# Kernel tuning notes

Measured on AMD Instinct MI355X. Metric: run time of the kernel, lower is better.

## Reference

```python
import jax, jax.numpy as jnp
import numpy as np

NUM_HEADS = 4
LOCAL_RADIUS = 2


def setup_inputs() -> dict:
    key = jax.random.key(0)
    ks = jax.random.split(key, 7)
    B, C, H, W = 1, 256, 40, 40
    O = 256  # out_channels
    s = 1.0 / np.sqrt(C).astype(np.float32)
    x = jax.random.normal(ks[0], (B, C, H, W), dtype=jnp.float32)
    Wq = jax.random.normal(ks[1], (C, O), dtype=jnp.float32) * s
    Wk = jax.random.normal(ks[2], (C, O), dtype=jnp.float32) * s
    Wv = jax.random.normal(ks[3], (C, O), dtype=jnp.float32) * s
    bq = jnp.zeros((O,), jnp.float32)
    bk = jnp.zeros((O,), jnp.float32)
    bv = jnp.zeros((O,), jnp.float32)
    return {"x": x, "Wq": Wq, "bq": bq, "Wk": Wk, "bk": bk, "Wv": Wv, "bv": bv}


def reference(x, Wq, bq, Wk, bk, Wv, bv):
    B, C, H, W = x.shape
    N = H * W
    O = Wq.shape[1]
    hd = O // NUM_HEADS
    # Faithful to torch: x.view(B, N, -1) is a raw row-major reshape of (B,C,H,W)
    xf = x.reshape(B, N, C)
    # projections -> (B, heads, N, head_dim)
    q = (xf @ Wq + bq).reshape(B, N, NUM_HEADS, hd).transpose(0, 2, 1, 3)
    k = (xf @ Wk + bk).reshape(B, N, NUM_HEADS, hd).transpose(0, 2, 1, 3)
    v = (xf @ Wv + bv).reshape(B, N, NUM_HEADS, hd).transpose(0, 2, 1, 3)
    scale = jnp.asarray(O, jnp.float32) ** 0.5
    acc = jnp.zeros_like(v)
    # 25 shifted full-attention passes; roll is over (heads, points) axes,
    # exactly matching torch key.roll(shifts=(h,w), dims=(-3,-2)).
    for h in range(-LOCAL_RADIUS, LOCAL_RADIUS + 1):
        for w in range(-LOCAL_RADIUS, LOCAL_RADIUS + 1):
            rk = jnp.roll(k, shift=(h, w), axis=(1, 2))
            scores = jnp.einsum('bhnd,bhmd->bhnm', q, rk) / scale  # (B,h,N,N)
            attn = jax.nn.softmax(scores, axis=-1)
            rv = jnp.roll(v, shift=(-h, -w), axis=(1, 2))
            acc = acc + jnp.einsum('bhnm,bhmd->bhnd', attn, rv)
    # (B, heads, N, hd) -> (B, N, O)
    return acc.transpose(0, 2, 1, 3).reshape(B, N, O)
```

## Files before the change

### kernel.cpp

```cpp
#include <hip/hip_runtime.h>
#include <hip/hip_bf16.h>
#include <stdint.h>

typedef __attribute__((ext_vector_type(8))) __bf16 bf16x8;
typedef __attribute__((ext_vector_type(4))) float f32x4;

#define N_PTS 1600
#define HD    64

#define OFF_WT   0u
#define OFF_BIAS 393216u
#define OFF_XS   394752u
#define OFF_QH   1213952u
#define OFF_KF   2033152u
#define OFF_VF   2852352u

__device__ __forceinline__ float bf2f(ushort h) {
  union { uint32_t u; float f; } v; v.u = ((uint32_t)h) << 16; return v.f;
}
__device__ __forceinline__ ushort f2bf(float f) {
  union { float f; uint32_t u; } v; v.f = f;
  uint32_t u = v.u;
  return (ushort)((u + 0x7FFFu + ((u >> 16) & 1u)) >> 16);
}
__device__ __forceinline__ uint32_t pk2(float a, float b) {
  union { __hip_bfloat162 h; uint32_t u; } cv;
  cv.h = __float22bfloat162_rn(make_float2(a, b));
  return cv.u;
}

__device__ __forceinline__ int detect_f32(const ushort* xu, int* shflag) {
  int t = threadIdx.x & 255;
  if (t == 0) *shflag = 0;
  __syncthreads();
  int local = 0;
#pragma unroll
  for (int i = 0; i < 4; ++i) {
    float v = bf2f(xu[(t * 4 + i) * 2]);
    if (!(fabsf(v) < 1e4f)) local = 1;
  }
  if (local) atomicOr(shflag, 1);
  __syncthreads();
  return *shflag;
}

__global__ void k_prep(const void* __restrict__ x, const void* __restrict__ Wq,
                       const void* __restrict__ bq, const void* __restrict__ Wk,
                       const void* __restrict__ bk, const void* __restrict__ Wv,
                       const void* __restrict__ bv, char* __restrict__ ws) {
  __shared__ int shflag;
  __shared__ ushort tileb[32][33];
  int isf32 = detect_f32((const ushort*)x, &shflag);
  int b = blockIdx.x, t = threadIdx.x;

  if (b < 192) {
    int z = b >> 6, tile = b & 63;
    const void* W = (z == 0) ? Wq : ((z == 1) ? Wk : Wv);
    int o0 = (tile & 7) * 32, k0 = (tile >> 3) * 32;
    int tx = t & 31, ty = t >> 5;
#pragma unroll
    for (int i = 0; i < 32; i += 8) {
      int kk = (k0 + ty + i) * 256 + o0 + tx;
      tileb[ty + i][tx] = isf32 ? f2bf(((const float*)W)[kk]) : ((const ushort*)W)[kk];
    }
    __syncthreads();
    ushort* WT = (ushort*)(ws + OFF_WT) + z * 65536;
#pragma unroll
    for (int i = 0; i < 32; i += 8)
      WT[(o0 + ty + i) * 256 + k0 + tx] = tileb[tx][ty + i];
  } else if (b == 192) {
    ushort* bb = (ushort*)(ws + OFF_BIAS);
#pragma unroll
    for (int z = 0; z < 3; ++z) {
      const void* B = (z == 0) ? bq : ((z == 1) ? bk : bv);
      bb[z * 256 + t] = isf32 ? f2bf(((const float*)B)[t]) : ((const ushort*)B)[t];
    }
  } else {
    int jid = (b - 193) * 256 + t;
    int n = jid >> 5, ch0 = (jid & 31) * 8;
    int nm4 = n - 4 + ((n < 4) ? 1600 : 0);
    int nm2 = n - 2 + ((n < 2) ? 1600 : 0);
    int np2 = n + 2 - ((n >= 1598) ? 1600 : 0);
    int np4 = n + 4 - ((n >= 1596) ? 1600 : 0);
    int rows[5] = {nm4, nm2, n, np2, np4};
    union { ushort us[8]; bf16x8 v; } rv[5];
    if (isf32) {
      const float4* X4 = (const float4*)x;
#pragma unroll
      for (int r = 0; r < 5; ++r) {
        int i4 = (rows[r] * 256 + ch0) >> 2;
        float4 f0 = X4[i4], f1 = X4[i4 + 1];
        rv[r].us[0] = f2bf(f0.x); rv[r].us[1] = f2bf(f0.y);
        rv[r].us[2] = f2bf(f0.z); rv[r].us[3] = f2bf(f0.w);
        rv[r].us[4] = f2bf(f1.x); rv[r].us[5] = f2bf(f1.y);
        rv[r].us[6] = f2bf(f1.z); rv[r].us[7] = f2bf(f1.w);
      }
    } else {
      const ushort* Xu = (const ushort*)x;
#pragma unroll
      for (int r = 0; r < 5; ++r)
        rv[r].v = *(const bf16x8*)(Xu + rows[r] * 256 + ch0);
    }
    union { ushort us[8]; bf16x8 v; } o;
#pragma unroll
    for (int j = 0; j < 8; ++j) {
      float s = bf2f(rv[0].us[j]) + bf2f(rv[1].us[j]) + bf2f(rv[2].us[j]) +
                bf2f(rv[3].us[j]) + bf2f(rv[4].us[j]);
      o.us[j] = f2bf(s);
    }
    *(bf16x8*)((ushort*)(ws + OFF_XS) + n * 256 + ch0) = o.v;
  }
}

__launch_bounds__(512)
__global__ void k_proj(const void* __restrict__ x, const ushort* __restrict__ WT,
                       const ushort* __restrict__ bias3, char* __restrict__ ws) {
  __shared__ int shflag;
  __shared__ ushort ktile[2][4][16][72];
  int isf32 = detect_f32((const ushort*)x, &shflag);
  int tid = threadIdx.x;
  int half = tid >> 8;
  int job = blockIdx.x + 150 * half;
  int z = job / 100, nb = job % 100;
  int n0 = nb * 16;
  const ushort* WTz = WT + z * 65536;
  const ushort* bias = bias3 + z * 256;
  int t256 = tid & 255;
  int head = t256 >> 6, lane = t256 & 63;
  int c = lane & 15, quad = lane >> 4;

  f32x4 acc[4];
#pragma unroll
  for (int i = 0; i < 4; ++i) acc[i] = (f32x4){0.f, 0.f, 0.f, 0.f};

  int ebase = (n0 + c) * 256;
  const ushort* Xs = (const ushort*)(ws + OFF_XS);
#pragma unroll
  for (int kt = 0; kt < 8; ++kt) {
    bf16x8 a;
    if (z == 2) {
      a = *(const bf16x8*)(Xs + ebase + kt * 32 + quad * 8);
    } else if (isf32) {
      const float4* X4 = (const float4*)x;
      int i4 = (ebase + kt * 32 + quad * 8) >> 2;
      float4 f0 = X4[i4], f1 = X4[i4 + 1];
      union { ushort us[8]; bf16x8 v; } cv;
      cv.us[0] = f2bf(f0.x); cv.us[1] = f2bf(f0.y);
      cv.us[2] = f2bf(f0.z); cv.us[3] = f2bf(f0.w);
      cv.us[4] = f2bf(f1.x); cv.us[5] = f2bf(f1.y);
      cv.us[6] = f2bf(f1.z); cv.us[7] = f2bf(f1.w);
      a = cv.v;
    } else {
      a = *(const bf16x8*)((const ushort*)x + ebase + kt * 32 + quad * 8);
    }
#pragma unroll
    for (int os = 0; os < 4; ++os) {
      bf16x8 bfr = *(const bf16x8*)(WTz + (head * 64 + os * 16 + c) * 256 + kt * 32 + quad * 8);
      acc[os] = __builtin_amdgcn_mfma_f32_16x16x32_bf16(a, bfr, acc[os], 0, 0, 0);
    }
  }

  float scale = (z == 0) ? 0.0625f * 1.44269504088896f : 1.0f;
  float bmul = (z == 2) ? 5.f : 1.f;
#pragma unroll
  for (int os = 0; os < 4; ++os) {
    float bval = bf2f(bias[head * 64 + os * 16 + c]);
#pragma unroll
    for (int r = 0; r < 4; ++r)
      ktile[half][head][quad * 4 + r][os * 16 + c] =
          f2bf((acc[os][r] + bmul * bval) * scale);
  }
  __syncthreads();

  if (z == 0) {
    ushort* Qh = (ushort*)(ws + OFF_QH);
    int kl = lane >> 2, d0 = (lane & 3) * 16;
    bf16x8 v0 = *(const bf16x8*)&ktile[half][head][kl][d0];
    bf16x8 v1 = *(const bf16x8*)&ktile[half][head][kl][d0 + 8];
    ushort* qrow = Qh + (size_t)head * (N_PTS * HD) + (size_t)(n0 + kl) * HD + d0;
    *(bf16x8*)qrow = v0;
    *(bf16x8*)(qrow + 8) = v1;
  } else if (z == 1) {
    ushort* Kf = (ushort*)(ws + OFF_KF);
    int hf = nb & 1, t = nb >> 1;
    int quad_o = lane >> 4, chp = (lane >> 3) & 1, cc = (lane & 7) + hf * 8;
#pragma unroll
    for (int e = 0; e < 2; ++e) {
      int ch = chp + 2 * e;
      int kl = ((cc >> 2) << 3) + (cc & 3) + ((ch >> 1) << 2) - hf * 16;
      int d0 = (ch & 1) * 32 + quad_o * 8;
      bf16x8 v = *(const bf16x8*)&ktile[half][head][kl][d0];
      *(bf16x8*)(Kf + ((((size_t)head * 50 + t) * 4 + ch) * 64 + quad_o * 16 + cc) * 8) = v;
    }
  } else {
    ushort* Vf = (ushort*)(ws + OFF_VF);
    int hf = nb & 1, t = nb >> 1;
    int cc = lane & 15, qh = (lane >> 4) & 1, dsp = lane >> 5;
#pragma unroll
    for (int e = 0; e < 2; ++e) {
      int ds = dsp * 2 + e;
      union { ushort us[8]; bf16x8 v; } o;
#pragma unroll
      for (int j = 0; j < 8; ++j)
        o.us[j] = ktile[half][head][8 * qh + j][ds * 16 + cc];
      *(bf16x8*)(Vf + ((((size_t)head * 50 + t) * 4 + ds) * 64 + (2 * hf + qh) * 16 + cc) * 8) = o.v;
    }
  }
}

__device__ __forceinline__ bf16x8 pack_p8(const f32x4& s0, const f32x4& s1, float& lp) {
  float e0 = exp2f(s0[0]), e1 = exp2f(s0[1]), e2 = exp2f(s0[2]), e3 = exp2f(s0[3]);
  float e4 = exp2f(s1[0]), e5 = exp2f(s1[1]), e6 = exp2f(s1[2]), e7 = exp2f(s1[3]);
  lp += ((e0 + e1) + (e2 + e3)) + ((e4 + e5) + (e6 + e7));
  union { uint32_t u[4]; bf16x8 v; } r;
  r.u[0] = pk2(e0, e1); r.u[1] = pk2(e2, e3);
  r.u[2] = pk2(e4, e5); r.u[3] = pk2(e6, e7);
  return r.v;
}

#define MFMA16(a, b, cc) __builtin_amdgcn_mfma_f32_16x16x32_bf16(a, b, cc, 0, 0, 0)

#define LOADT(sfx, t) do {                                            \
    const char* kt_ = kfp + (size_t)(t) * 4096;                       \
    const char* vt_ = vfp + (size_t)(t) * 4096;                       \
    ka0##sfx = *(const bf16x8*)(kt_);                                 \
    ka1##sfx = *(const bf16x8*)(kt_ + 1024);                          \
    kb0##sfx = *(const bf16x8*)(kt_ + 2048);                          \
    kb1##sfx = *(const bf16x8*)(kt_ + 3072);                          \
    vb0##sfx = *(const bf16x8*)(vt_);                                 \
    vb1##sfx = *(const bf16x8*)(vt_ + 1024);                          \
    vb2##sfx = *(const bf16x8*)(vt_ + 2048);                          \
    vb3##sfx = *(const bf16x8*)(vt_ + 3072);                          \
  } while (0)

#define COMPUTE(sfx) do {                                             \
    __builtin_amdgcn_s_setprio(1);                                    \
    f32x4 s0 = MFMA16(ka0##sfx, qa00, z4);                            \
    s0 = MFMA16(ka1##sfx, qa01, s0);                                  \
    f32x4 s1 = MFMA16(kb0##sfx, qa00, z4);                            \
    s1 = MFMA16(kb1##sfx, qa01, s1);                                  \
    bf16x8 pa0 = pack_p8(s0, s1, lp0);                                \
    oacc0[0] = MFMA16(pa0, vb0##sfx, oacc0[0]);                       \
    oacc0[1] = MFMA16(pa0, vb1##sfx, oacc0[1]);                       \
    oacc0[2] = MFMA16(pa0, vb2##sfx, oacc0[2]);                       \
    oacc0[3] = MFMA16(pa0, vb3##sfx, oacc0[3]);                       \
    s0 = MFMA16(ka0##sfx, qa10, z4);                                  \
    s0 = MFMA16(ka1##sfx, qa11, s0);                                  \
    s1 = MFMA16(kb0##sfx, qa10, z4);                                  \
    s1 = MFMA16(kb1##sfx, qa11, s1);                                  \
    bf16x8 pa1 = pack_p8(s0, s1, lp1);                                \
    oacc1[0] = MFMA16(pa1, vb0##sfx, oacc1[0]);                       \
    oacc1[1] = MFMA16(pa1, vb1##sfx, oacc1[1]);                       \
    oacc1[2] = MFMA16(pa1, vb2##sfx, oacc1[2]);                       \
    oacc1[3] = MFMA16(pa1, vb3##sfx, oacc1[3]);                       \
    __builtin_amdgcn_s_setprio(0);                                    \
  } while (0)

__launch_bounds__(512)
__global__ void k_attn(const ushort* __restrict__ Qh, const ushort* __restrict__ Kf,
                       const ushort* __restrict__ Vf, const void* __restrict__ x,
                       void* __restrict__ out) {
  __shared__ int shflag;
  __shared__ float obuf[8][16][68];
  __shared__ float lbuf[8][16];
  int isf32 = detect_f32((const ushort*)x, &shflag);

  int qt = blockIdx.x;
  int hp = blockIdx.y;
  int tid = threadIdx.x, sp = tid >> 6, lane = tid & 63;
  int kg = sp & 3, zh = sp >> 2;
  int vg = (2 * hp - kg + 8) & 3;
  int c = lane & 15, quad = lane >> 4;
  int n0 = qt * 16;

  const ushort* q0row = Qh + ((hp    ) * N_PTS + n0 + c) * HD;
  const ushort* q1row = Qh + ((hp + 2) * N_PTS + n0 + c) * HD;
  bf16x8 qa00 = *(const bf16x8*)(q0row + quad * 8);
  bf16x8 qa01 = *(const bf16x8*)(q0row + 32 + quad * 8);
  bf16x8 qa10 = *(const bf16x8*)(q1row + quad * 8);
  bf16x8 qa11 = *(const bf16x8*)(q1row + 32 + quad * 8);

  f32x4 oacc0[4], oacc1[4];
#pragma unroll
  for (int i = 0; i < 4; ++i) {
    oacc0[i] = (f32x4){0.f, 0.f, 0.f, 0.f};
    oacc1[i] = (f32x4){0.f, 0.f, 0.f, 0.f};
  }
  float lp0 = 0.f, lp1 = 0.f;

  int off = zh * 25;
  const int iters = 25;
  const f32x4 z4 = (f32x4){0.f, 0.f, 0.f, 0.f};

  const char* kfp = (const char*)Kf + (size_t)(kg * 50 + off) * 4096 + lane * 16;
  const char* vfp = (const char*)Vf + (size_t)(vg * 50 + off) * 4096 + lane * 16;

  bf16x8 ka0A, ka1A, kb0A, kb1A, vb0A, vb1A, vb2A, vb3A;
  bf16x8 ka0B, ka1B, kb0B, kb1B, vb0B, vb1B, vb2B, vb3B;

  LOADT(A, 0);
  int it = 0;
  for (; it + 2 <= iters; it += 2) {
    LOADT(B, it + 1);
    COMPUTE(A);
    int tn = (it + 2 < iters) ? (it + 2) : (it + 1);
    LOADT(A, tn);
    COMPUTE(B);
  }
  if (it < iters) COMPUTE(A);

  lp0 += __shfl_xor(lp0, 16, 64); lp0 += __shfl_xor(lp0, 32, 64);
  lp1 += __shfl_xor(lp1, 16, 64); lp1 += __shfl_xor(lp1, 32, 64);

#pragma unroll
  for (int h = 0; h < 2; ++h) {
    __syncthreads();
    const f32x4* oa = h ? oacc1 : oacc0;
#pragma unroll
    for (int ds = 0; ds < 4; ++ds)
#pragma unroll
      for (int r = 0; r < 4; ++r)
        obuf[sp][quad * 4 + r][ds * 16 + c] = oa[ds][r];
    if (quad == 0) lbuf[sp][c] = h ? lp1 : lp0;
    __syncthreads();

    int q = tid >> 5, dp = (tid & 31) * 2;
    int hq = hp + 2 * h;
    float a0 = 0.f, a1 = 0.f;
#pragma unroll
    for (int g = 0; g < 4; ++g) {
      float n0v = obuf[g][q][dp]     + obuf[g + 4][q][dp];
      float n1v = obuf[g][q][dp + 1] + obuf[g + 4][q][dp + 1];
      float l   = lbuf[g][q] + lbuf[g + 4][q];
      float w   = (g == ((hq + 2) & 3)) ? 2.f : 1.f;
      float rl  = w / l;
      a0 += n0v * rl; a1 += n1v * rl;
    }
    size_t oidx = (size_t)(n0 + q) * 256 + hq * 64 + dp;
    if (isf32) {
      ((float2*)out)[oidx >> 1] = make_float2(a0, a1);
    } else {
      ((uint32_t*)out)[oidx >> 1] = pk2(a0, a1);
    }
  }
}

extern "C" void kernel_launch(void* const* d_in, const int* in_sizes, int n_in,
                              void* d_out, int out_size, void* d_ws, size_t ws_size,
                              hipStream_t stream) {
  char* ws = (char*)d_ws;
  ushort* WT    = (ushort*)(ws + OFF_WT);
  ushort* bias3 = (ushort*)(ws + OFF_BIAS);
  ushort* Qh    = (ushort*)(ws + OFF_QH);
  ushort* Kf    = (ushort*)(ws + OFF_KF);
  ushort* Vf    = (ushort*)(ws + OFF_VF);

  k_prep<<<393, 256, 0, stream>>>(d_in[0], d_in[1], d_in[2], d_in[3],
                                  d_in[4], d_in[5], d_in[6], ws);
  k_proj<<<150, 512, 0, stream>>>(d_in[0], WT, bias3, ws);
  k_attn<<<dim3(100, 2), 512, 0, stream>>>(Qh, Kf, Vf, d_in[0], d_out);
}
```

Before: 106.5 us.

## Split projection kernel into per-head blocks for more parallelism

The projection kernel now launches 1200 blocks of 256 threads, one per (matrix, head, 16-row tile), instead of 150 blocks of 512 threads each computing four heads. Each wave computes a single 16x16 output tile rather than four, which spreads the work over far more CUs on a chip with many compute units. In exchange, each block reloads its 16-row activation tile, so activation reads are repeated four times. The scatter phase also leaves half the threads idle for the K and V layouts.

```diff
diff --git a/kernel.cpp b/kernel.cpp
--- a/kernel.cpp
+++ b/kernel.cpp
@@ -112,29 +112,26 @@
   }
 }
 
-__launch_bounds__(512)
+__launch_bounds__(256)
 __global__ void k_proj(const void* __restrict__ x, const ushort* __restrict__ WT,
                        const ushort* __restrict__ bias3, char* __restrict__ ws) {
   __shared__ int shflag;
-  __shared__ ushort ktile[2][4][16][72];
+  __shared__ ushort ktile[16][72];
   int isf32 = detect_f32((const ushort*)x, &shflag);
-  int tid = threadIdx.x;
-  int half = tid >> 8;
-  int job = blockIdx.x + 150 * half;
-  int z = job / 100, nb = job % 100;
+  int b = blockIdx.x;
+  int z = b / 400, rem = b % 400;
+  int head = rem / 100, nb = rem % 100;
   int n0 = nb * 16;
   const ushort* WTz = WT + z * 65536;
   const ushort* bias = bias3 + z * 256;
-  int t256 = tid & 255;
-  int head = t256 >> 6, lane = t256 & 63;
+  int tid = threadIdx.x;
+  int os = tid >> 6, lane = tid & 63;
   int c = lane & 15, quad = lane >> 4;
 
-  f32x4 acc[4];
-#pragma unroll
-  for (int i = 0; i < 4; ++i) acc[i] = (f32x4){0.f, 0.f, 0.f, 0.f};
-
+  f32x4 acc = (f32x4){0.f, 0.f, 0.f, 0.f};
   int ebase = (n0 + c) * 256;
   const ushort* Xs = (const ushort*)(ws + OFF_XS);
+  const ushort* wrow = WTz + (head * 64 + os * 16 + c) * 256;
 #pragma unroll
   for (int kt = 0; kt < 8; ++kt) {
     bf16x8 a;
@@ -153,56 +150,42 @@
     } else {
       a = *(const bf16x8*)((const ushort*)x + ebase + kt * 32 + quad * 8);
     }
-#pragma unroll
-    for (int os = 0; os < 4; ++os) {
-      bf16x8 bfr = *(const bf16x8*)(WTz + (head * 64 + os * 16 + c) * 256 + kt * 32 + quad * 8);
-      acc[os] = __builtin_amdgcn_mfma_f32_16x16x32_bf16(a, bfr, acc[os], 0, 0, 0);
-    }
+    bf16x8 bfr = *(const bf16x8*)(wrow + kt * 32 + quad * 8);
+    acc = __builtin_amdgcn_mfma_f32_16x16x32_bf16(a, bfr, acc, 0, 0, 0);
   }
 
   float scale = (z == 0) ? 0.0625f * 1.44269504088896f : 1.0f;
   float bmul = (z == 2) ? 5.f : 1.f;
-#pragma unroll
-  for (int os = 0; os < 4; ++os) {
-    float bval = bf2f(bias[head * 64 + os * 16 + c]);
-#pragma unroll
-    for (int r = 0; r < 4; ++r)
-      ktile[half][head][quad * 4 + r][os * 16 + c] =
-          f2bf((acc[os][r] + bmul * bval) * scale);
-  }
+  float bval = bf2f(bias[head * 64 + os * 16 + c]);
+#pragma unroll
+  for (int r = 0; r < 4; ++r)
+    ktile[quad * 4 + r][os * 16 + c] = f2bf((acc[r] + bmul * bval) * scale);
   __syncthreads();
 
   if (z == 0) {
     ushort* Qh = (ushort*)(ws + OFF_QH);
-    int kl = lane >> 2, d0 = (lane & 3) * 16;
-    bf16x8 v0 = *(const bf16x8*)&ktile[half][head][kl][d0];
-    bf16x8 v1 = *(const bf16x8*)&ktile[half][head][kl][d0 + 8];
-    ushort* qrow = Qh + (size_t)head * (N_PTS * HD) + (size_t)(n0 + kl) * HD + d0;
-    *(bf16x8*)qrow = v0;
-    *(bf16x8*)(qrow + 8) = v1;
+    int kl = tid >> 4, d4 = (tid & 15) * 4;
+    ushort4 v = *(const ushort4*)&ktile[kl][d4];
+    *(ushort4*)(Qh + (size_t)head * (N_PTS * HD) + (size_t)(n0 + kl) * HD + d4) = v;
   } else if (z == 1) {
-    ushort* Kf = (ushort*)(ws + OFF_KF);
-    int hf = nb & 1, t = nb >> 1;
-    int quad_o = lane >> 4, chp = (lane >> 3) & 1, cc = (lane & 7) + hf * 8;
-#pragma unroll
-    for (int e = 0; e < 2; ++e) {
-      int ch = chp + 2 * e;
+    if (tid < 128) {
+      ushort* Kf = (ushort*)(ws + OFF_KF);
+      int hf = nb & 1, t = nb >> 1;
+      int quad_o = tid >> 5, ch = (tid >> 3) & 3, cc = (tid & 7) + hf * 8;
       int kl = ((cc >> 2) << 3) + (cc & 3) + ((ch >> 1) << 2) - hf * 16;
       int d0 = (ch & 1) * 32 + quad_o * 8;
-      bf16x8 v = *(const bf16x8*)&ktile[half][head][kl][d0];
+      bf16x8 v = *(const bf16x8*)&ktile[kl][d0];
       *(bf16x8*)(Kf + ((((size_t)head * 50 + t) * 4 + ch) * 64 + quad_o * 16 + cc) * 8) = v;
     }
   } else {
-    ushort* Vf = (ushort*)(ws + OFF_VF);
-    int hf = nb & 1, t = nb >> 1;
-    int cc = lane & 15, qh = (lane >> 4) & 1, dsp = lane >> 5;
-#pragma unroll
-    for (int e = 0; e < 2; ++e) {
-      int ds = dsp * 2 + e;
+    if (tid < 128) {
+      ushort* Vf = (ushort*)(ws + OFF_VF);
+      int hf = nb & 1, t = nb >> 1;
+      int ds = tid >> 5, qh = (tid >> 4) & 1, cc = tid & 15;
       union { ushort us[8]; bf16x8 v; } o;
 #pragma unroll
       for (int j = 0; j < 8; ++j)
-        o.us[j] = ktile[half][head][8 * qh + j][ds * 16 + cc];
+        o.us[j] = ktile[8 * qh + j][ds * 16 + cc];
       *(bf16x8*)(Vf + ((((size_t)head * 50 + t) * 4 + ds) * 64 + (2 * hf + qh) * 16 + cc) * 8) = o.v;
     }
   }
@@ -357,6 +340,6 @@
 
   k_prep<<<393, 256, 0, stream>>>(d_in[0], d_in[1], d_in[2], d_in[3],
                                   d_in[4], d_in[5], d_in[6], ws);
-  k_proj<<<150, 512, 0, stream>>>(d_in[0], WT, bias3, ws);
+  k_proj<<<1200, 256, 0, stream>>>(d_in[0], WT, bias3, ws);
   k_attn<<<dim3(100, 2), 512, 0, stream>>>(Qh, Kf, Vf, d_in[0], d_out);
 }
```

Result: slower. 109.6 us (+2.8%).
